# Performance work log

Hardware: AMD Instinct MI355X
Metric: run time of the kernel (lower is better)

Reference implementation:

```python
import jax, jax.numpy as jnp
import numpy as np

B = 2
IMG = (128, 256, 256)
P = 16
E, NH, DH = 768, 12, 64
L, F = 12, 3072
WS = (512, 1024, 2048)   # LongNet segment lengths
RS = (1, 2, 4)           # matching dilation ratios
NEG = -1e9
NPATCH = (IMG[0] // P) * (IMG[1] // P) * (IMG[2] // P)
S = NPATCH + 1           # +1 CLS token


def setup_inputs() -> dict:
    key = jax.random.key(0)
    ks = jax.random.split(key, 16)
    def nrm(k, shape, std=0.02):
        return jax.random.normal(k, shape, jnp.float32) * std
    return {
        "x": jax.random.normal(ks[0], (B, 1) + IMG, jnp.float32),
        "conv_w": nrm(ks[1], (E, 1, P, P, P)),
        "conv_b": jnp.zeros((E,), jnp.float32),
        "cls_token": nrm(ks[2], (1, 1, E)),
        "pos_embed": nrm(ks[3], (1, S, E)),
        "ln1_g": jnp.ones((L, E)), "ln1_b": jnp.zeros((L, E)),
        "wq": nrm(ks[4], (L, E, E)), "bq": jnp.zeros((L, E)),
        "wk": nrm(ks[5], (L, E, E)), "bk": jnp.zeros((L, E)),
        "wv": nrm(ks[6], (L, E, E)), "bv": jnp.zeros((L, E)),
        "wo": nrm(ks[7], (L, E, E)), "bo": jnp.zeros((L, E)),
        "ln2_g": jnp.ones((L, E)), "ln2_b": jnp.zeros((L, E)),
        "w1": nrm(ks[8], (L, E, F)), "b1": jnp.zeros((L, F)),
        "w2": nrm(ks[9], (L, F, E)), "b2": jnp.zeros((L, E)),
        "normf_g": jnp.ones((E,)), "normf_b": jnp.zeros((E,)),
    }


def _ln(x, g, b, eps=1e-5):
    m = x.mean(-1, keepdims=True)
    v = ((x - m) ** 2).mean(-1, keepdims=True)
    return (x - m) * jax.lax.rsqrt(v + eps) * g + b


def _dilated_branch(q, k, v, w, r):
    # LongNet dilated attention for one (segment_length w, dilation r) config.
    # q,k,v: [B,S,H,d]. Head h uses offset h % r inside each segment of length w.
    b, s0, h, d = q.shape
    sp = -(-s0 // w) * w
    pad = sp - s0
    qp, kp, vp = (jnp.pad(t, ((0, 0), (0, pad), (0, 0), (0, 0))) for t in (q, k, v))
    n, m = sp // w, w // r
    idx = (jnp.arange(h)[:, None] % r) + jnp.arange(m)[None, :] * r      # [h,m]
    seg = lambda t: t.reshape(b, n, w, h, d).transpose(0, 1, 3, 2, 4)    # [b,n,h,w,d]
    gidx = idx[None, None, :, :, None]
    qs = jnp.take_along_axis(seg(qp), gidx, axis=3)                      # [b,n,h,m,d]
    ks = jnp.take_along_axis(seg(kp), gidx, axis=3)
    vs = jnp.take_along_axis(seg(vp), gidx, axis=3)
    kvalid = (jnp.arange(sp) < s0).reshape(n, w)[:, idx]                 # [n,h,m]
    scores = jnp.einsum('bnhqd,bnhkd->bnhqk', qs, ks) * (d ** -0.5)
    scores = jnp.where(kvalid[None, :, :, None, :], scores, NEG)
    lse = jax.nn.logsumexp(scores, axis=-1)                              # [b,n,h,m]
    out = jnp.einsum('bnhqk,bnhkd->bnhqd', jax.nn.softmax(scores, -1), vs)
    hh = jnp.arange(h)[:, None]
    out_f = jnp.zeros((b, n, h, w, d), q.dtype).at[:, :, hh, idx, :].set(out)
    lse_f = jnp.full((b, n, h, w), NEG, q.dtype).at[:, :, hh, idx].set(lse)
    return (out_f.transpose(0, 1, 3, 2, 4).reshape(b, sp, h, d),
            lse_f.transpose(0, 1, 3, 2).reshape(b, sp, h))


def _dilated_attention(q, k, v):
    # Combine branches weighted by softmax normalizers (exp lse), per LongNet.
    b, s0, h, d = q.shape
    smax = max(-(-s0 // w) * w for w in WS)
    outs, lses = [], []
    for w, r in zip(WS, RS):
        o, l = _dilated_branch(q, k, v, w, r)
        outs.append(jnp.pad(o, ((0, 0), (0, smax - o.shape[1]), (0, 0), (0, 0))))
        lses.append(jnp.pad(l, ((0, 0), (0, smax - l.shape[1]), (0, 0)),
                            constant_values=NEG))
    wgt = jax.nn.softmax(jnp.stack(lses), axis=0)[..., None]             # [nb,b,smax,h,1]
    out = (wgt * jnp.stack(outs)).sum(0)                                 # [b,smax,h,d]
    return out[:, :s0]


def reference(x, conv_w, conv_b, cls_token, pos_embed, ln1_g, ln1_b, wq, bq,
              wk, bk, wv, bv, wo, bo, ln2_g, ln2_b, w1, b1, w2, b2,
              normf_g, normf_b):
    b = x.shape[0]
    dp, hp, wp = IMG[0] // P, IMG[1] // P, IMG[2] // P
    # Conv3d patch embed with stride == kernel -> block reshape + matmul
    xp = x.reshape(b, 1, dp, P, hp, P, wp, P).transpose(0, 2, 4, 6, 1, 3, 5, 7)
    xp = xp.reshape(b, dp * hp * wp, -1) @ conv_w.reshape(E, -1).T + conv_b
    h = jnp.concatenate([jnp.broadcast_to(cls_token, (b, 1, E)), xp], axis=1)
    h = h + pos_embed  # seq length matches pos_embed, no interpolation needed

    def layer(hst, p):
        g1, lb1, Wq, Bq, Wk, Bk, Wv, Bv, Wo, Bo, g2, lb2, W1, B1, W2, B2 = p
        y = _ln(hst, g1, lb1)
        q = (y @ Wq + Bq).reshape(b, S, NH, DH)
        k = (y @ Wk + Bk).reshape(b, S, NH, DH)
        v = (y @ Wv + Bv).reshape(b, S, NH, DH)
        a = _dilated_attention(q, k, v).reshape(b, S, E) @ Wo + Bo
        hst = hst + a
        y = _ln(hst, g2, lb2)
        hst = hst + jax.nn.gelu(y @ W1 + B1, approximate=False) @ W2 + B2
        return hst, None

    params = (ln1_g, ln1_b, wq, bq, wk, bk, wv, bv, wo, bo,
              ln2_g, ln2_b, w1, b1, w2, b2)
    h, _ = jax.lax.scan(layer, h, params)
    h = _ln(h, normf_g, normf_b)
    return h[:, 0]
```

## Files before the change

kernel.cpp:

```cpp
#include <hip/hip_runtime.h>
#include <math.h>

#define SEQ 2049
#define EMB 768
#define NHEADS 12
#define QKVW 2304
#define MROWS 4098
#define MPAD 4224
#define NEGV -1000000000.0f

typedef short bs8 __attribute__((ext_vector_type(8)));
typedef float f4 __attribute__((ext_vector_type(4)));

__device__ __forceinline__ unsigned short f2bf(float f){
  union { float f; unsigned u; } x; x.f = f;
  unsigned r = x.u + 0x7fffu + ((x.u >> 16) & 1u);
  return (unsigned short)(r >> 16);
}
__device__ __forceinline__ float bf2f(unsigned short u){
  union { unsigned u; float f; } x; x.u = ((unsigned)u) << 16; return x.f;
}

__device__ __forceinline__ void gl_lds16(const void* g, void* l){
  __builtin_amdgcn_global_load_lds((const __attribute__((address_space(1))) void*)g,
                                   (__attribute__((address_space(3))) void*)l, 16, 0, 0);
}

__global__ void wtr_k(const float* __restrict__ src, unsigned short* __restrict__ dst,
                      int K, int N, int LD, int NOFF)
{
  __shared__ float tile[32][33];
  int k0 = blockIdx.x*32, n0 = blockIdx.y*32, z = blockIdx.z;
  int tx = threadIdx.x, ty = threadIdx.y;
  const float* s = src + (size_t)z*K*N;
#pragma unroll
  for (int i=0;i<4;++i)
    tile[ty*4+i][tx] = s[(size_t)(k0+ty*4+i)*N + n0+tx];
  __syncthreads();
  unsigned short* dz = dst + ((size_t)z*LD + NOFF)*K;
#pragma unroll
  for (int i=0;i<4;++i)
    dz[(size_t)(n0+ty*4+i)*K + k0+tx] = f2bf(tile[tx][ty*4+i]);
}

__global__ void castconv_k(const float* __restrict__ src, unsigned short* __restrict__ dst){
  size_t i = ((size_t)blockIdx.x*256 + threadIdx.x)*4;
  float4 f = *(const float4*)(src+i);
  dst[i+0]=f2bf(f.x); dst[i+1]=f2bf(f.y); dst[i+2]=f2bf(f.z); dst[i+3]=f2bf(f.w);
}

__global__ void biascat_k(const float* __restrict__ bq, const float* __restrict__ bk,
                          const float* __restrict__ bv, float* __restrict__ dst){
  int i = blockIdx.x*256+threadIdx.x;
  int l = i/QKVW, c = i%QKVW;
  float v = (c<768) ? bq[l*768+c] : (c<1536 ? bk[l*768+c-768] : bv[l*768+c-1536]);
  dst[i] = v;
}

__global__ void patchify_k(const float* __restrict__ x, unsigned short* __restrict__ Xp)
{
  size_t gid = (size_t)blockIdx.x*256 + threadIdx.x;
  size_t oi = gid*4;
  int row = (int)(oi >> 12);
  int c = (int)(oi & 4095);
  int b = row >> 11; int p = row & 2047;
  int pd = p >> 8, ph = (p>>4)&15, pw = p&15;
  int pz = c >> 8, py = (c>>4)&15, px = c&15;
  size_t src = (((size_t)(b*128 + pd*16+pz)*256) + (size_t)(ph*16+py))*256 + (size_t)(pw*16+px);
  float4 f = *(const float4*)(x+src);
  Xp[oi+0]=f2bf(f.x); Xp[oi+1]=f2bf(f.y); Xp[oi+2]=f2bf(f.z); Xp[oi+3]=f2bf(f.w);
}

__global__ void assemble_k(const float* __restrict__ P, size_t pstride,
                           const float* __restrict__ cls,
                           const float* __restrict__ pos_e, float* __restrict__ H)
{
  int row = blockIdx.x; int t = threadIdx.x;
  float* hr = H + (size_t)row*EMB;
  if (row >= MROWS) { hr[t]=0.f; hr[t+256]=0.f; hr[t+512]=0.f; return; }
  int b = row / SEQ; int pos = row - b*SEQ;
#pragma unroll
  for (int c0=0;c0<3;++c0) {
    int c = t + c0*256;
    float v;
    if (pos==0) v = cls[c];
    else {
      size_t idx = ((size_t)(b*2048 + pos-1))*EMB + c;
      v = P[idx] + P[pstride+idx] + P[2*pstride+idx] + P[3*pstride+idx];
    }
    hr[c] = v + pos_e[(size_t)pos*EMB + c];
  }
}

__global__ __launch_bounds__(256) void ln_k(const float* __restrict__ H,
    const float* __restrict__ gam, const float* __restrict__ bet,
    unsigned short* __restrict__ Y)
{
  int row = blockIdx.x, t = threadIdx.x;
  const float* hr = H + (size_t)row*EMB;
  float v0 = hr[t], v1 = hr[t+256], v2 = hr[t+512];
  float s = v0+v1+v2;
#pragma unroll
  for (int off=32; off>=1; off>>=1) s += __shfl_down(s, off);
  __shared__ float r1[4], r2[4];
  if ((t&63)==0) r1[t>>6] = s;
  __syncthreads();
  float mean = (r1[0]+r1[1]+r1[2]+r1[3]) * (1.f/768.f);
  float d0=v0-mean, d1=v1-mean, d2=v2-mean;
  float q = d0*d0+d1*d1+d2*d2;
#pragma unroll
  for (int off=32; off>=1; off>>=1) q += __shfl_down(q, off);
  if ((t&63)==0) r2[t>>6] = q;
  __syncthreads();
  float rstd = rsqrtf((r2[0]+r2[1]+r2[2]+r2[3])*(1.f/768.f) + 1e-5f);
  unsigned short* yr = Y + (size_t)row*EMB;
  yr[t]     = f2bf(d0*rstd*gam[t]     + bet[t]);
  yr[t+256] = f2bf(d1*rstd*gam[t+256] + bet[t+256]);
  yr[t+512] = f2bf(d2*rstd*gam[t+512] + bet[t+512]);
}

template<int S>
__global__ __launch_bounds__(256) void ln_red_k(float* __restrict__ H,
    const float* __restrict__ P, size_t pstride,
    const float* __restrict__ gam, const float* __restrict__ bet,
    unsigned short* __restrict__ Y)
{
  int row = blockIdx.x, t = threadIdx.x;
  size_t base = (size_t)row*EMB;
  float v[3];
#pragma unroll
  for (int c0=0;c0<3;++c0) {
    size_t idx = base + t + c0*256;
    float h = H[idx];
#pragma unroll
    for (int s=0;s<S;++s) h += P[(size_t)s*pstride + idx];
    H[idx] = h; v[c0] = h;
  }
  float s = v[0]+v[1]+v[2];
#pragma unroll
  for (int off=32; off>=1; off>>=1) s += __shfl_down(s, off);
  __shared__ float r1[4], r2[4];
  if ((t&63)==0) r1[t>>6] = s;
  __syncthreads();
  float mean = (r1[0]+r1[1]+r1[2]+r1[3]) * (1.f/768.f);
  float d0=v[0]-mean, d1=v[1]-mean, d2=v[2]-mean;
  float q = d0*d0+d1*d1+d2*d2;
#pragma unroll
  for (int off=32; off>=1; off>>=1) q += __shfl_down(q, off);
  if ((t&63)==0) r2[t>>6] = q;
  __syncthreads();
  float rstd = rsqrtf((r2[0]+r2[1]+r2[2]+r2[3])*(1.f/768.f) + 1e-5f);
  unsigned short* yr = Y + base;
  yr[t]     = f2bf(d0*rstd*gam[t]     + bet[t]);
  yr[t+256] = f2bf(d1*rstd*gam[t+256] + bet[t+256]);
  yr[t+512] = f2bf(d2*rstd*gam[t+512] + bet[t+512]);
}

__global__ __launch_bounds__(256) void final_ln_red_k(const float* __restrict__ H,
   const float* __restrict__ P, size_t pstride,
   const float* __restrict__ gam, const float* __restrict__ bet, float* __restrict__ out)
{
  int b = blockIdx.x, t = threadIdx.x;
  size_t base = (size_t)(b*SEQ)*EMB;
  float v[3];
#pragma unroll
  for (int c0=0;c0<3;++c0) {
    size_t idx = base + t + c0*256;
    float h = H[idx];
#pragma unroll
    for (int s=0;s<4;++s) h += P[(size_t)s*pstride + idx];
    v[c0] = h;
  }
  float s = v[0]+v[1]+v[2];
#pragma unroll
  for (int off=32; off>=1; off>>=1) s += __shfl_down(s, off);
  __shared__ float r1[4], r2[4];
  if ((t&63)==0) r1[t>>6] = s;
  __syncthreads();
  float mean = (r1[0]+r1[1]+r1[2]+r1[3]) * (1.f/768.f);
  float d0=v[0]-mean, d1=v[1]-mean, d2=v[2]-mean;
  float q = d0*d0+d1*d1+d2*d2;
#pragma unroll
  for (int off=32; off>=1; off>>=1) q += __shfl_down(q, off);
  if ((t&63)==0) r2[t>>6] = q;
  __syncthreads();
  float rstd = rsqrtf((r2[0]+r2[1]+r2[2]+r2[3])*(1.f/768.f) + 1e-5f);
  out[b*EMB + t]     = d0*rstd*gam[t]     + bet[t];
  out[b*EMB + t+256] = d1*rstd*gam[t+256] + bet[t+256];
  out[b*EMB + t+512] = d2*rstd*gam[t+512] + bet[t+512];
}

template<int MODE, int NSPLIT>
__global__ __launch_bounds__(256) void gemm_k(
    const unsigned short* __restrict__ A,
    const unsigned short* __restrict__ Bt,
    const float* __restrict__ bias,
    unsigned short* __restrict__ Cb,
    float* __restrict__ Cf,
    int K, int ldc, size_t splitStride)
{
  __shared__ __attribute__((aligned(16))) unsigned short lA[128*32];
  __shared__ __attribute__((aligned(16))) unsigned short lB[128*32];
  const int tid = threadIdx.x;
  const int w = tid>>6, lane = tid&63, g = lane>>4, l16 = lane&15;
  const int lr = lane>>2, lc = (lane&3)*8;
  const int nwg = gridDim.x*gridDim.y;
  const int id = blockIdx.y*gridDim.x + blockIdx.x;
  const int q = nwg>>3, r = nwg&7, xc = id&7, si = id>>3;
  const int nid = (xc<r ? xc*(q+1) : r*(q+1)+(xc-r)*q) + si;
  const int tm = nid / gridDim.x;
  const int tn = nid - tm*gridDim.x;
  const int kchunk = K / NSPLIT;
  const int kofs = (NSPLIT>1) ? blockIdx.z * kchunk : 0;
  const unsigned short* Ab = A + (size_t)tm*128*K + kofs;
  const unsigned short* Bb = Bt + (size_t)tn*128*K + kofs;
  const int wm = (w>>1)*64, wn = (w&1)*64;
  f4 acc[4][4] = {};
  const int nkt = kchunk>>5;
  for (int kt=0; kt<nkt; ++kt) {
    __syncthreads();
    const size_t ko = (size_t)(kt*32 + lc);
    gl_lds16(Ab + (size_t)(w*16 + lr)*K + ko,     ((char*)lA) + w*1024);
    gl_lds16(Ab + (size_t)((w+4)*16 + lr)*K + ko, ((char*)lA) + (w+4)*1024);
    gl_lds16(Bb + (size_t)(w*16 + lr)*K + ko,     ((char*)lB) + w*1024);
    gl_lds16(Bb + (size_t)((w+4)*16 + lr)*K + ko, ((char*)lB) + (w+4)*1024);
    __syncthreads();
    bs8 af[4], bf[4];
#pragma unroll
    for (int mi=0;mi<4;++mi) af[mi] = *(const bs8*)(lA + (wm+mi*16+l16)*32 + g*8);
#pragma unroll
    for (int ni=0;ni<4;++ni) bf[ni] = *(const bs8*)(lB + (wn+ni*16+l16)*32 + g*8);
#pragma unroll
    for (int mi=0;mi<4;++mi)
#pragma unroll
      for (int ni=0;ni<4;++ni)
        acc[mi][ni] = __builtin_amdgcn_mfma_f32_16x16x32_bf16(af[mi], bf[ni], acc[mi][ni], 0,0,0);
  }
  const float bscale = (NSPLIT==1 || blockIdx.z==0) ? 1.f : 0.f;
#pragma unroll
  for (int mi=0;mi<4;++mi)
#pragma unroll
    for (int ni=0;ni<4;++ni) {
      int col = tn*128 + wn + ni*16 + l16;
      float bv = bias[col]*bscale;
#pragma unroll
      for (int r0=0;r0<4;++r0) {
        int row = tm*128 + wm + mi*16 + g*4 + r0;
        float val = acc[mi][ni][r0] + bv;
        if (MODE==1) val = 0.5f*val*(1.f+erff(val*0.70710678f));
        if (MODE<=1) Cb[(size_t)row*ldc + col] = f2bf(val);
        else Cf[(size_t)blockIdx.z*splitStride + (size_t)row*ldc + col] = val;
      }
    }
}

__global__ __launch_bounds__(256) void attn_all_k(
    const unsigned short* __restrict__ qkv,
    unsigned short* __restrict__ O1, float* __restrict__ L1,
    unsigned short* __restrict__ O2, float* __restrict__ L2,
    unsigned short* __restrict__ O3, float* __restrict__ L3)
{
  __shared__ __attribute__((aligned(16))) unsigned short lK[128*72];
  __shared__ __attribute__((aligned(16))) unsigned short lVt[64*136];
  __shared__ __attribute__((aligned(16))) unsigned short Pl[4][16][136];
  const int tid = threadIdx.x;
  const int w = tid>>6, lane = tid&63, g = lane>>4, l16 = lane&15;

  int id = blockIdx.x;
  int R, WSZ, NSEG; unsigned short* OB; float* LB;
  if (id < 960)       { R=1; WSZ=512;  NSEG=5; OB=O1; LB=L1; }
  else if (id < 1536) { id -= 960;  R=2; WSZ=1024; NSEG=3; OB=O2; LB=L2; }
  else                { id -= 1536; R=4; WSZ=2048; NSEG=2; OB=O3; LB=L3; }
  const int qt = id & 7; int rest = id >> 3;
  const int seg = rest % NSEG; const int bh = rest / NSEG;
  const int b = bh / NHEADS, hd = bh % NHEADS;
  const int hr = hd % R;
  const int j0 = qt*64 + w*16;
  const int kbase = seg*WSZ + hr;
  const unsigned short* qkvb = qkv + (size_t)b*SEQ*QKVW;

  bs8 z = {0,0,0,0,0,0,0,0};
  bs8 qf0 = z, qf1 = z;
  {
    int qpos = kbase + (j0 + l16)*R;
    if (qpos < SEQ) {
      const unsigned short* qrow = qkvb + (size_t)qpos*QKVW + hd*64 + g*8;
      qf0 = *(const bs8*)(qrow);
      qf1 = *(const bs8*)(qrow + 32);
    }
  }

  float rm[4], rs[4];
  f4 oacc[4] = {};
#pragma unroll
  for (int r=0;r<4;++r) { rm[r] = NEGV; rs[r] = 0.f; }

  for (int c=0; c<4; ++c) {
    __syncthreads();
#pragma unroll
    for (int it=0; it<4; ++it) {
      int idx = tid + it*256;
      int kk = idx >> 3, dblk = idx & 7;
      int kpos = kbase + (c*128 + kk)*R;
      bs8 kv = z;
      if (kpos < SEQ) kv = *(const bs8*)(qkvb + (size_t)kpos*QKVW + EMB + hd*64 + dblk*8);
      *(bs8*)(lK + kk*72 + dblk*8) = kv;
    }
#pragma unroll
    for (int it=0; it<4; ++it) {
      int idx = tid + it*256;
      int kk = idx & 127, dblk = idx >> 7;
      int kpos = kbase + (c*128 + kk)*R;
      unsigned short tv[8] = {0,0,0,0,0,0,0,0};
      if (kpos < SEQ)
        *(bs8*)tv = *(const bs8*)(qkvb + (size_t)kpos*QKVW + 1536 + hd*64 + dblk*8);
#pragma unroll
      for (int ii=0; ii<8; ++ii) lVt[(dblk*8+ii)*136 + kk] = tv[ii];
    }
    __syncthreads();

    f4 sc[8];
#pragma unroll
    for (int kt=0; kt<8; ++kt) {
      int key = kt*16 + l16;
      bs8 kf0 = *(const bs8*)(lK + key*72 + g*8);
      bs8 kf1 = *(const bs8*)(lK + key*72 + 32 + g*8);
      f4 acc = {0.f,0.f,0.f,0.f};
      acc = __builtin_amdgcn_mfma_f32_16x16x32_bf16(qf0, kf0, acc, 0,0,0);
      acc = __builtin_amdgcn_mfma_f32_16x16x32_bf16(qf1, kf1, acc, 0,0,0);
      int kpos = kbase + (c*128 + key)*R;
      bool kvld = (kpos < SEQ);
#pragma unroll
      for (int r=0;r<4;++r) sc[kt][r] = kvld ? acc[r]*0.125f : NEGV;
    }
    float scl[4];
#pragma unroll
    for (int r=0;r<4;++r) {
      float mx = sc[0][r];
#pragma unroll
      for (int kt=1;kt<8;++kt) mx = fmaxf(mx, sc[kt][r]);
      mx = fmaxf(mx, __shfl_xor(mx, 1));
      mx = fmaxf(mx, __shfl_xor(mx, 2));
      mx = fmaxf(mx, __shfl_xor(mx, 4));
      mx = fmaxf(mx, __shfl_xor(mx, 8));
      float mn = fmaxf(rm[r], mx);
      scl[r] = __expf(rm[r] - mn);
      rm[r] = mn;
    }
#pragma unroll
    for (int r=0;r<4;++r) {
      float sm = 0.f;
#pragma unroll
      for (int kt=0;kt<8;++kt) { float p = __expf(sc[kt][r] - rm[r]); sc[kt][r] = p; sm += p; }
      sm += __shfl_xor(sm, 1); sm += __shfl_xor(sm, 2);
      sm += __shfl_xor(sm, 4); sm += __shfl_xor(sm, 8);
      rs[r] = rs[r]*scl[r] + sm;
    }
#pragma unroll
    for (int dt=0; dt<4; ++dt)
#pragma unroll
      for (int r=0;r<4;++r) oacc[dt][r] *= scl[r];
#pragma unroll
    for (int kt=0;kt<8;++kt)
#pragma unroll
      for (int r=0;r<4;++r)
        Pl[w][g*4+r][kt*16+l16] = f2bf(sc[kt][r]);
#pragma unroll
    for (int ks=0; ks<4; ++ks) {
      bs8 pa = *(const bs8*)(&Pl[w][l16][ks*32 + g*8]);
#pragma unroll
      for (int dt=0; dt<4; ++dt) {
        bs8 vb = *(const bs8*)(lVt + (dt*16+l16)*136 + ks*32 + g*8);
        oacc[dt] = __builtin_amdgcn_mfma_f32_16x16x32_bf16(pa, vb, oacc[dt], 0,0,0);
      }
    }
  }

  size_t obase = ((size_t)(b*NSEG + seg)*NHEADS + hd)*512;
#pragma unroll
  for (int dt=0; dt<4; ++dt)
#pragma unroll
    for (int r=0;r<4;++r) {
      int j = j0 + g*4 + r;
      OB[(obase + j)*64 + dt*16 + l16] = f2bf(oacc[dt][r] / rs[r]);
    }
  if (l16 == 0) {
#pragma unroll
    for (int r=0;r<4;++r) LB[obase + j0 + g*4 + r] = rm[r] + __logf(rs[r]);
  }
}

__global__ __launch_bounds__(256) void attn_combine_k(
   const unsigned short* __restrict__ o1, const float* __restrict__ l1,
   const unsigned short* __restrict__ o2, const float* __restrict__ l2,
   const unsigned short* __restrict__ o3, const float* __restrict__ l3,
   unsigned short* __restrict__ attn)
{
  int row = blockIdx.x; int t = threadIdx.x;
  unsigned short* arow = attn + (size_t)row*EMB;
  if (row >= MROWS) { arow[t]=0; arow[t+256]=0; arow[t+512]=0; return; }
  int b = row / SEQ, pos = row - (row/SEQ)*SEQ;
#pragma unroll
  for (int c0=0; c0<3; ++c0) {
    int cc = t + c0*256;
    int hd = cc >> 6, d = cc & 63;
    float L0,L1v,L2v,O0,O1v,O2v;
    {
      int seg = pos >> 9; int j = pos & 511;
      size_t base = ((size_t)(b*5 + seg)*NHEADS + hd)*512 + j;
      L0 = l1[base]; O0 = bf2f(o1[base*64 + d]);
    }
    if ((pos & 1) == (hd & 1)) {
      int seg = pos >> 10; int j = ((pos & 1023) - (hd&1)) >> 1;
      size_t base = ((size_t)(b*3 + seg)*NHEADS + hd)*512 + j;
      L1v = l2[base]; O1v = bf2f(o2[base*64 + d]);
    } else { L1v = NEGV; O1v = 0.f; }
    if ((pos & 3) == (hd & 3)) {
      int seg = pos >> 11; int j = ((pos & 2047) - (hd&3)) >> 2;
      size_t base = ((size_t)(b*2 + seg)*NHEADS + hd)*512 + j;
      L2v = l3[base]; O2v = bf2f(o3[base*64 + d]);
    } else { L2v = NEGV; O2v = 0.f; }
    float m = fmaxf(L0, fmaxf(L1v, L2v));
    float e0 = __expf(L0-m), e1 = __expf(L1v-m), e2 = __expf(L2v-m);
    float inv = 1.f/(e0+e1+e2);
    arow[cc] = f2bf((e0*O0+e1*O1v+e2*O2v)*inv);
  }
}

extern "C" void kernel_launch(void* const* d_in, const int* in_sizes, int n_in,
                              void* d_out, int out_size, void* d_ws, size_t ws_size,
                              hipStream_t stream) {
  const float* x       = (const float*)d_in[0];
  const float* conv_w  = (const float*)d_in[1];
  const float* conv_b  = (const float*)d_in[2];
  const float* cls     = (const float*)d_in[3];
  const float* pos_e   = (const float*)d_in[4];
  const float* ln1_g   = (const float*)d_in[5];
  const float* ln1_b   = (const float*)d_in[6];
  const float* wq      = (const float*)d_in[7];
  const float* bq      = (const float*)d_in[8];
  const float* wk      = (const float*)d_in[9];
  const float* bk      = (const float*)d_in[10];
  const float* wv      = (const float*)d_in[11];
  const float* bv      = (const float*)d_in[12];
  const float* wo      = (const float*)d_in[13];
  const float* bo      = (const float*)d_in[14];
  const float* ln2_g   = (const float*)d_in[15];
  const float* ln2_b   = (const float*)d_in[16];
  const float* w1      = (const float*)d_in[17];
  const float* b1      = (const float*)d_in[18];
  const float* w2      = (const float*)d_in[19];
  const float* b2      = (const float*)d_in[20];
  const float* nf_g    = (const float*)d_in[21];
  const float* nf_b    = (const float*)d_in[22];

  char* ws = (char*)d_ws;
  size_t off = 0;
  auto alloc = [&](size_t bytes)->char* {
    char* p = ws + off; off += (bytes + 255) & ~(size_t)255; return p;
  };
  unsigned short* wqkv_t = (unsigned short*)alloc((size_t)12*2304*768*2);
  unsigned short* wo_t   = (unsigned short*)alloc((size_t)12*768*768*2);
  unsigned short* w1_t   = (unsigned short*)alloc((size_t)12*3072*768*2);
  unsigned short* w2_t   = (unsigned short*)alloc((size_t)12*768*3072*2);
  unsigned short* cw_b   = (unsigned short*)alloc((size_t)768*4096*2);
  float* bqkv            = (float*)alloc((size_t)12*2304*4);
  unsigned short* Xp     = (unsigned short*)alloc((size_t)4096*4096*2);
  float* H               = (float*)alloc((size_t)MPAD*768*4);
  float* P               = (float*)alloc((size_t)4*MPAD*768*4);
  unsigned short* Y      = (unsigned short*)alloc((size_t)MPAD*768*2);
  unsigned short* QKV    = (unsigned short*)alloc((size_t)MPAD*2304*2);
  unsigned short* ATT    = (unsigned short*)alloc((size_t)MPAD*768*2);
  unsigned short* Y2     = (unsigned short*)alloc((size_t)MPAD*3072*2);
  unsigned short* O1 = (unsigned short*)alloc((size_t)2*5*12*512*64*2);
  unsigned short* O2 = (unsigned short*)alloc((size_t)2*3*12*512*64*2);
  unsigned short* O3 = (unsigned short*)alloc((size_t)2*2*12*512*64*2);
  float* L1 = (float*)alloc((size_t)2*5*12*512*4);
  float* L2 = (float*)alloc((size_t)2*3*12*512*4);
  float* L3 = (float*)alloc((size_t)2*2*12*512*4);
  const size_t PSTR = (size_t)MPAD*768;

  dim3 tb(32,8);
  wtr_k<<<dim3(24,24,12), tb, 0, stream>>>(wq, wqkv_t, 768, 768, 2304, 0);
  wtr_k<<<dim3(24,24,12), tb, 0, stream>>>(wk, wqkv_t, 768, 768, 2304, 768);
  wtr_k<<<dim3(24,24,12), tb, 0, stream>>>(wv, wqkv_t, 768, 768, 2304, 1536);
  wtr_k<<<dim3(24,24,12), tb, 0, stream>>>(wo, wo_t, 768, 768, 768, 0);
  wtr_k<<<dim3(24,96,12), tb, 0, stream>>>(w1, w1_t, 768, 3072, 3072, 0);
  wtr_k<<<dim3(96,24,12), tb, 0, stream>>>(w2, w2_t, 3072, 768, 768, 0);
  castconv_k<<<3072,256,0,stream>>>(conv_w, cw_b);
  biascat_k<<<108,256,0,stream>>>(bq,bk,bv,bqkv);
  patchify_k<<<16384,256,0,stream>>>(x, Xp);
  gemm_k<3,4><<<dim3(6,32,4),256,0,stream>>>(Xp, cw_b, conv_b, nullptr, P, 4096, 768, PSTR);
  assemble_k<<<MPAD,256,0,stream>>>(P, PSTR, cls, pos_e, H);

  for (int l=0;l<12;++l) {
    if (l==0) ln_k<<<MPAD,256,0,stream>>>(H, ln1_g, ln1_b, Y);
    else ln_red_k<4><<<MPAD,256,0,stream>>>(H, P, PSTR, ln1_g + l*768, ln1_b + l*768, Y);
    gemm_k<0,1><<<dim3(18,33),256,0,stream>>>(Y, wqkv_t + (size_t)l*2304*768, bqkv + l*2304, QKV, nullptr, 768, 2304, 0);
    attn_all_k<<<1920,256,0,stream>>>(QKV, O1,L1,O2,L2,O3,L3);
    attn_combine_k<<<MPAD,256,0,stream>>>(O1,L1,O2,L2,O3,L3, ATT);
    gemm_k<3,2><<<dim3(6,33,2),256,0,stream>>>(ATT, wo_t + (size_t)l*768*768, bo + l*768, nullptr, P, 768, 768, PSTR);
    ln_red_k<2><<<MPAD,256,0,stream>>>(H, P, PSTR, ln2_g + l*768, ln2_b + l*768, Y);
    gemm_k<1,1><<<dim3(24,33),256,0,stream>>>(Y, w1_t + (size_t)l*3072*768, b1 + l*3072, Y2, nullptr, 768, 3072, 0);
    gemm_k<3,4><<<dim3(6,33,4),256,0,stream>>>(Y2, w2_t + (size_t)l*768*3072, b2 + l*768, nullptr, P, 3072, 768, PSTR);
  }
  final_ln_red_k<<<2,256,0,stream>>>(H, P, PSTR, nf_g, nf_b, (float*)d_out);
}
```

Measured before the change: 3.213 ms.

## Double-buffer GEMM LDS tiles and XOR-swizzle columns to cut bank conflicts

The bf16 MFMA GEMM now uses two LDS buffers, so the global-to-LDS load of the next K tile is issued before the current tile is consumed, with explicit vmcnt waits and barriers. The global source column is XOR-swizzled by row and the LDS reads apply the matching swizzle, which is meant to reduce LDS bank conflicts on the fragment loads. This doubles LDS use per block, which can lower occupancy, and adds a second barrier per iteration after the fragment reads.

```diff
diff --git a/kernel.cpp b/kernel.cpp
--- a/kernel.cpp
+++ b/kernel.cpp
@@ -199,11 +199,13 @@
     float* __restrict__ Cf,
     int K, int ldc, size_t splitStride)
 {
-  __shared__ __attribute__((aligned(16))) unsigned short lA[128*32];
-  __shared__ __attribute__((aligned(16))) unsigned short lB[128*32];
+  __shared__ __attribute__((aligned(16))) unsigned short lA[2][128*32];
+  __shared__ __attribute__((aligned(16))) unsigned short lB[2][128*32];
   const int tid = threadIdx.x;
   const int w = tid>>6, lane = tid&63, g = lane>>4, l16 = lane&15;
-  const int lr = lane>>2, lc = (lane&3)*8;
+  const int lr = lane>>2;
+  const int lcs = (((lane&3) ^ ((lane>>3)&3)))*8;
+  const int swz = ((g ^ ((l16>>1)&3)))*8;
   const int nwg = gridDim.x*gridDim.y;
   const int id = blockIdx.y*gridDim.x + blockIdx.x;
   const int q = nwg>>3, r = nwg&7, xc = id&7, si = id>>3;
@@ -217,24 +219,40 @@
   const int wm = (w>>1)*64, wn = (w&1)*64;
   f4 acc[4][4] = {};
   const int nkt = kchunk>>5;
+
+  auto STAGE = [&](int buf, int kt){
+    const size_t ko = (size_t)(kt*32 + lcs);
+    gl_lds16(Ab + (size_t)(w*16 + lr)*K + ko,     ((char*)lA[buf]) + w*1024);
+    gl_lds16(Ab + (size_t)((w+4)*16 + lr)*K + ko, ((char*)lA[buf]) + (w+4)*1024);
+    gl_lds16(Bb + (size_t)(w*16 + lr)*K + ko,     ((char*)lB[buf]) + w*1024);
+    gl_lds16(Bb + (size_t)((w+4)*16 + lr)*K + ko, ((char*)lB[buf]) + (w+4)*1024);
+  };
+
+  STAGE(0, 0);
+  int cur = 0;
   for (int kt=0; kt<nkt; ++kt) {
-    __syncthreads();
-    const size_t ko = (size_t)(kt*32 + lc);
-    gl_lds16(Ab + (size_t)(w*16 + lr)*K + ko,     ((char*)lA) + w*1024);
-    gl_lds16(Ab + (size_t)((w+4)*16 + lr)*K + ko, ((char*)lA) + (w+4)*1024);
-    gl_lds16(Bb + (size_t)(w*16 + lr)*K + ko,     ((char*)lB) + w*1024);
-    gl_lds16(Bb + (size_t)((w+4)*16 + lr)*K + ko, ((char*)lB) + (w+4)*1024);
-    __syncthreads();
+    if (kt+1 < nkt) {
+      STAGE(cur^1, kt+1);
+      asm volatile("s_waitcnt vmcnt(4)" ::: "memory");
+    } else {
+      asm volatile("s_waitcnt vmcnt(0)" ::: "memory");
+    }
+    __builtin_amdgcn_sched_barrier(0);
+    __builtin_amdgcn_s_barrier();
     bs8 af[4], bf[4];
 #pragma unroll
-    for (int mi=0;mi<4;++mi) af[mi] = *(const bs8*)(lA + (wm+mi*16+l16)*32 + g*8);
-#pragma unroll
-    for (int ni=0;ni<4;++ni) bf[ni] = *(const bs8*)(lB + (wn+ni*16+l16)*32 + g*8);
+    for (int mi=0;mi<4;++mi) af[mi] = *(const bs8*)(lA[cur] + (wm+mi*16+l16)*32 + swz);
+#pragma unroll
+    for (int ni=0;ni<4;++ni) bf[ni] = *(const bs8*)(lB[cur] + (wn+ni*16+l16)*32 + swz);
+    asm volatile("s_waitcnt lgkmcnt(0)" ::: "memory");
+    __builtin_amdgcn_sched_barrier(0);
+    __builtin_amdgcn_s_barrier();
 #pragma unroll
     for (int mi=0;mi<4;++mi)
 #pragma unroll
       for (int ni=0;ni<4;++ni)
         acc[mi][ni] = __builtin_amdgcn_mfma_f32_16x16x32_bf16(af[mi], bf[ni], acc[mi][ni], 0,0,0);
+    cur ^= 1;
   }
   const float bscale = (NSPLIT==1 || blockIdx.z==0) ? 1.f : 0.f;
 #pragma unroll
```

Result: faster. 3.063 ms (-4.7%).
